# Kernel tuning notes

Measured on AMD Instinct MI355X. Metric: run time of the kernel, lower is better.

Reference implementation:

```python
import jax, jax.numpy as jnp
import numpy as np
import math

B, N, IN_DIM = 128, 100, 8
E, H, FF, L = 512, 8, 2048, 6
DH = E // H
MAX_STEPS = int(N * 1.5)
EPS = 1e-5

def _ln(x, g, b):
    mu = x.mean(-1, keepdims=True)
    var = ((x - mu) ** 2).mean(-1, keepdims=True)
    return (x - mu) / jnp.sqrt(var + EPS) * g + b

def _mha(q_in, k_in, v_in, wq, bq, wk, bk, wv, bv, wo, bo):
    Bq, Sq = q_in.shape[0], q_in.shape[1]
    q = (q_in @ wq + bq).reshape(Bq, Sq, H, DH)
    k = (k_in @ wk + bk).reshape(Bq, -1, H, DH)
    v = (v_in @ wv + bv).reshape(Bq, -1, H, DH)
    s = jnp.einsum('bqhd,bkhd->bhqk', q, k) / math.sqrt(DH)
    a = jax.nn.softmax(s, axis=-1)
    o = jnp.einsum('bhqk,bkhd->bqhd', a, v).reshape(Bq, Sq, E)
    return o @ wo + bo

def setup_inputs():
    key = jax.random.key(0)
    keys = iter(jax.random.split(key, 64))
    def nrm(shape, s=0.02):
        return jax.random.normal(next(keys), shape, jnp.float32) * s
    d = {}
    d['node_features'] = jax.random.normal(next(keys), (B, N, IN_DIM), jnp.float32)
    d['edge_weights'] = jax.random.uniform(next(keys), (B, N, N), jnp.float32)
    pos = np.arange(N)[:, None].astype(np.float32)
    div = np.exp(np.arange(0, E, 2).astype(np.float32) * (-math.log(10000.0) / E))
    pe = np.zeros((N, E), np.float32)
    pe[:, 0::2] = np.sin(pos * div); pe[:, 1::2] = np.cos(pos * div)
    d['pe'] = jnp.asarray(pe)
    d['in_w'] = nrm((IN_DIM, E)); d['in_b'] = jnp.zeros((E,), jnp.float32)
    for nm in ['enc_wq', 'enc_wk', 'enc_wv', 'enc_wo']:
        d[nm] = nrm((L, E, E))
    for nm in ['enc_bq', 'enc_bk', 'enc_bv', 'enc_bo']:
        d[nm] = jnp.zeros((L, E), jnp.float32)
    d['enc_w1'] = nrm((L, E, FF)); d['enc_b1'] = jnp.zeros((L, FF), jnp.float32)
    d['enc_w2'] = nrm((L, FF, E)); d['enc_b2'] = jnp.zeros((L, E), jnp.float32)
    d['enc_ln1g'] = jnp.ones((L, E), jnp.float32); d['enc_ln1b'] = jnp.zeros((L, E), jnp.float32)
    d['enc_ln2g'] = jnp.ones((L, E), jnp.float32); d['enc_ln2b'] = jnp.zeros((L, E), jnp.float32)
    d['lstm_wih'] = nrm((E, 4 * E)); d['lstm_whh'] = nrm((E, 4 * E))
    d['lstm_bih'] = jnp.zeros((4 * E,), jnp.float32); d['lstm_bhh'] = jnp.zeros((4 * E,), jnp.float32)
    for nm in ['dec_wq', 'dec_wk', 'dec_wv', 'dec_wo', 'dec_pw']:
        d[nm] = nrm((E, E))
    for nm in ['dec_bq', 'dec_bk', 'dec_bv', 'dec_bo', 'dec_pb']:
        d[nm] = jnp.zeros((E,), jnp.float32)
    d['dec_lng'] = jnp.ones((E,), jnp.float32); d['dec_lnb'] = jnp.zeros((E,), jnp.float32)
    d['shortcut_bonus'] = jnp.asarray(5.0, jnp.float32)
    d['revisit_penalty'] = jnp.asarray(-0.5, jnp.float32)
    d['done_w'] = nrm((E, 1)); d['done_b'] = jnp.zeros((1,), jnp.float32)
    return d

def _forward(node_features, edge_weights, pe, in_w, in_b, enc_wq, enc_bq, enc_wk, enc_bk, enc_wv, enc_bv, enc_wo, enc_bo, enc_w1, enc_b1, enc_w2, enc_b2, enc_ln1g, enc_ln1b, enc_ln2g, enc_ln2b, lstm_wih, lstm_whh, lstm_bih, lstm_bhh, dec_wq, dec_bq, dec_wk, dec_bk, dec_wv, dec_bv, dec_wo, dec_bo, dec_pw, dec_pb, dec_lng, dec_lnb, shortcut_bonus, revisit_penalty, done_w, done_b):
    # ---- Encoder (dropout = eval-mode identity) ----
    x = node_features @ in_w + in_b + pe[:N]
    for l in range(L):
        attn = _mha(x, x, x, enc_wq[l], enc_bq[l], enc_wk[l], enc_bk[l], enc_wv[l], enc_bv[l], enc_wo[l], enc_bo[l])
        x = _ln(x + attn, enc_ln1g[l], enc_ln1b[l])
        ff = jax.nn.relu(x @ enc_w1[l] + enc_b1[l]) @ enc_w2[l] + enc_b2[l]
        x = _ln(x + ff, enc_ln2g[l], enc_ln2b[l])
    node_emb = x  # [B, N, E]

    ar = jnp.arange(N)
    ew_to_first = edge_weights[:, :, 0]  # dist(mid -> node 0), [B, N]

    def step_fn(carry, step):
        h, c, ctx, visited, ucount, complete, all_vis, first, prev = carry
        # LSTMCell, torch gate order (i, f, g, o)
        gates = ctx @ lstm_wih + lstm_bih + h @ lstm_whh + lstm_bhh
        i_g, f_g, g_g, o_g = jnp.split(gates, 4, axis=-1)
        c2 = jax.nn.sigmoid(f_g) * c + jax.nn.sigmoid(i_g) * jnp.tanh(g_g)
        h2 = jax.nn.sigmoid(o_g) * jnp.tanh(c2)
        # greedy done-predictor: stop if sigmoid(logit) > 0.5 once tour can be closed
        done_p = jax.nn.sigmoid(h2 @ done_w + done_b)[:, 0]
        eligible = (~complete) & (ucount >= N) & (step >= N)
        complete = complete | (eligible & (done_p > 0.5))
        # DecoderStep: 1-query attention over node embeddings
        a = _mha(h2[:, None, :], node_emb, node_emb, dec_wq, dec_bq, dec_wk, dec_bk, dec_wv, dec_bv, dec_wo, dec_bo)[:, 0]
        a = _ln(a, dec_lng, dec_lnb)
        logits = a @ dec_pw + dec_pb
        scores = jnp.einsum('be,bne->bn', logits, node_emb)
        # revisit penalty while tour incomplete (vectorized masked_fill_)
        scores = jnp.where((~all_vis)[:, None] & visited, revisit_penalty, scores)
        # shortcut bonus once all nodes visited (vectorized gather over edge_weights)
        ew_prev = jnp.take_along_axis(edge_weights, prev[:, None, None], axis=1)[:, 0, :]  # [B, N] row dist(prev -> *)
        direct = ew_prev[:, :1]                      # dist(prev -> 0)
        via = ew_prev + ew_to_first                  # dist(prev -> mid) + dist(mid -> 0)
        bonus = jnp.where(via < direct, shortcut_bonus * (direct - via) / direct, 0.0)
        scores = scores + jnp.where(all_vis[:, None], bonus, 0.0)
        # completed tours: force return to first node
        scores = jnp.where(complete[:, None], -1e9, scores)
        scores = jnp.where(complete[:, None] & (ar[None, :] == first[:, None]), 100.0, scores)
        probs = jax.nn.softmax(scores, axis=1)
        curr = jnp.argmax(probs, axis=1).astype(jnp.int32)  # greedy selection
        logp = jnp.log(jnp.take_along_axis(probs, curr[:, None], 1)[:, 0] + 1e-10)
        first = jnp.where(step == 0, curr, first)
        # state updates (guarded by active, as in the torch per-batch loop)
        active = ~complete
        cur_mask = ar[None, :] == curr[:, None]
        newly = active & ~jnp.take_along_axis(visited, curr[:, None], 1)[:, 0]
        ucount = ucount + newly.astype(jnp.int32)
        visited = visited | (active[:, None] & cur_mask)
        all_vis = all_vis | (ucount >= N)
        ctx2 = jnp.take_along_axis(node_emb, curr[:, None, None], axis=1)[:, 0, :]
        return (h2, c2, ctx2, visited, ucount, complete, all_vis, first, curr), (curr, logp)

    carry0 = (jnp.zeros((B, E), jnp.float32), jnp.zeros((B, E), jnp.float32), node_emb.mean(1),
              jnp.zeros((B, N), bool), jnp.zeros((B,), jnp.int32),
              jnp.zeros((B,), bool), jnp.zeros((B,), bool),
              jnp.zeros((B,), jnp.int32), jnp.zeros((B,), jnp.int32))
    carry, (tours, logps) = jax.lax.scan(step_fn, carry0, jnp.arange(MAX_STEPS))
    complete, first = carry[5], carry[7]
    # final forced step (step == max_steps in torch): incomplete tours return to first node, logp = 0
    final_node = jnp.where(complete, jnp.int32(0), first)
    tours = jnp.concatenate([tours, final_node[None]], 0)                 # [MAX_STEPS+1, B]
    logps = jnp.concatenate([logps, jnp.zeros((1, B), jnp.float32)], 0)   # [MAX_STEPS+1, B]
    return logps, tours

def reference(node_features, edge_weights, pe, in_w, in_b, enc_wq, enc_bq, enc_wk, enc_bk, enc_wv, enc_bv, enc_wo, enc_bo, enc_w1, enc_b1, enc_w2, enc_b2, enc_ln1g, enc_ln1b, enc_ln2g, enc_ln2b, lstm_wih, lstm_whh, lstm_bih, lstm_bhh, dec_wq, dec_bq, dec_wk, dec_bk, dec_wv, dec_bv, dec_wo, dec_bo, dec_pw, dec_pb, dec_lng, dec_lnb, shortcut_bonus, revisit_penalty, done_w, done_b):
    return _forward(node_features, edge_weights, pe, in_w, in_b, enc_wq, enc_bq, enc_wk, enc_bk, enc_wv, enc_bv, enc_wo, enc_bo, enc_w1, enc_b1, enc_w2, enc_b2, enc_ln1g, enc_ln1b, enc_ln2g, enc_ln2b, lstm_wih, lstm_whh, lstm_bih, lstm_bhh, dec_wq, dec_bq, dec_wk, dec_bk, dec_wv, dec_bv, dec_wo, dec_bo, dec_pw, dec_pb, dec_lng, dec_lnb, shortcut_bonus, revisit_penalty, done_w, done_b)
```

## Files before the change

### kernel.cpp

```cpp
#include <hip/hip_runtime.h>
#include <math.h>

#define Bb 128
#define Nn 100
#define Ee 512
#define Hh 8
#define DHd 64
#define FFf 2048
#define Ll 6
#define STEPS 150

typedef _Float16 h8 __attribute__((ext_vector_type(8)));
typedef _Float16 h4 __attribute__((ext_vector_type(4)));
typedef float f4 __attribute__((ext_vector_type(4)));

template<bool RELU, bool BIAS, bool OUTF32, bool SPLITK>
__global__ __launch_bounds__(256) void mgemm_k(
    const _Float16* __restrict__ Ah, const _Float16* __restrict__ Al, int lda,
    const _Float16* __restrict__ Bh, const _Float16* __restrict__ Bl, int ldb,
    float* __restrict__ C, _Float16* __restrict__ Ch, _Float16* __restrict__ Cl,
    int ldc, const float* __restrict__ bias, int K, int kc, int Mtot)
{
  __shared__ _Float16 sm[4 * 5120];
  _Float16* sAh = sm;
// ... 96 lines not shown
  *(h4*)(Th + (size_t)(n0 + r) * K + k0 + c4) = hi;
  *(h4*)(Tl + (size_t)(n0 + r) * K + k0 + c4) = lo;
}

__global__ __launch_bounds__(256) void reduce4_k(
    const float* __restrict__ P, const float* __restrict__ bias, float* __restrict__ out)
{
  int idx = blockIdx.x * 256 + threadIdx.x;
  const size_t S = 3200ull * 512;
  float v = P[idx] + P[idx + S] + P[idx + 2 * S] + P[idx + 3 * S] + bias[idx & 511];
  out[idx] = v;
}

__global__ __launch_bounds__(256) void input_proj_k(
    const float* __restrict__ nf, const float* __restrict__ inw,
    const float* __restrict__ inb, const float* __restrict__ pe,
    float* __restrict__ x, _Float16* __restrict__ xh, _Float16* __restrict__ xl)
{
  int idx = blockIdx.x * 256 + threadIdx.x;
  int bn = idx >> 9, e = idx & 511;
  int n = bn - (bn / Nn) * Nn;
  const float* fr = nf + (size_t)bn * 8;
  float s = inb[e] + pe[(size_t)n * 512 + e];
#pragma unroll
  for (int i = 0; i < 8; ++i) s += fr[i] * inw[(size_t)i * 512 + e];
  x[idx] = s;
  _Float16 hh = (_Float16)s;
  xh[idx] = hh;
  xl[idx] = (_Float16)(s - (float)hh);
}

__global__ __launch_bounds__(256) void ln_k(
    const float* __restrict__ xin, const float* __restrict__ yin,
    const float* __restrict__ g, const float* __restrict__ bb,
    float* __restrict__ out, _Float16* __restrict__ oh, _Float16* __restrict__ ol)
{
  int row = blockIdx.x, t = threadIdx.x;
  __shared__ float red[256];
  size_t base = (size_t)row * 512;
  float v0 = xin[base + t] + yin[base + t];
  float v1 = xin[base + 256 + t] + yin[base + 256 + t];
  red[t] = v0 + v1;
  __syncthreads();
  for (int o = 128; o > 0; o >>= 1) { if (t < o) red[t] += red[t + o]; __syncthreads(); }
  float mu = red[0] * (1.f / 512.f);
  __syncthreads();
  float d0 = v0 - mu, d1 = v1 - mu;
  red[t] = d0 * d0 + d1 * d1;
  __syncthreads();
  for (int o = 128; o > 0; o >>= 1) { if (t < o) red[t] += red[t + o]; __syncthreads(); }
  float inv = 1.f / sqrtf(red[0] * (1.f / 512.f) + 1e-5f);
  float y0 = d0 * inv * g[t] + bb[t];
  float y1 = d1 * inv * g[t + 256] + bb[t + 256];
  out[base + t] = y0;
  out[base + 256 + t] = y1;
  _Float16 h0 = (_Float16)y0, h1 = (_Float16)y1;
  oh[base + t] = h0;           ol[base + t] = (_Float16)(y0 - (float)h0);
  oh[base + 256 + t] = h1;     ol[base + 256 + t] = (_Float16)(y1 - (float)h1);
}

__global__ __launch_bounds__(256) void enc_attn_k(
    const float* __restrict__ q, const float* __restrict__ k,
    const float* __restrict__ v, _Float16* __restrict__ oh, _Float16* __restrict__ ol)
{
  __shared__ __align__(16) float smem[14848];
  int bh = blockIdx.x; int b = bh >> 3, h = bh & 7;
  int t = threadIdx.x;
  float* qs = smem;
  float* kT = smem + 7616;
  float* p  = smem;
  const float* qg = q + ((size_t)b * Nn) * 512 + h * 64;
  const float* kg = k + ((size_t)b * Nn) * 512 + h * 64;
  const float* vg = v + ((size_t)b * Nn) * 512 + h * 64;
  for (int idx = t; idx < 6400; idx += 256) {
    int i = idx >> 6, d = idx & 63;
    qs[i * 68 + d]  = qg[(size_t)i * 512 + d];
    kT[d * 113 + i] = kg[(size_t)i * 512 + d];
  }
  __syncthreads();
  int ti = t >> 4, tj = t & 15;
  int i0 = ti * 7, j0 = tj * 7;
  float s[7][7];
#pragma unroll
  for (int r = 0; r < 7; ++r)
#pragma unroll
    for (int c = 0; c < 7; ++c) s[r][c] = 0.f;
  for (int kk = 0; kk < 64; ++kk) {
    float a[7], bb[7];
#pragma unroll
    for (int r = 0; r < 7; ++r) a[r] = qs[(i0 + r) * 68 + kk];
#pragma unroll
    for (int c = 0; c < 7; ++c) bb[c] = kT[kk * 113 + j0 + c];
#pragma unroll
    for (int r = 0; r < 7; ++r)
#pragma unroll
      for (int c = 0; c < 7; ++c) s[r][c] += a[r] * bb[c];
  }
  __syncthreads();
#pragma unroll
  for (int r = 0; r < 7; ++r)
#pragma unroll
    for (int c = 0; c < 7; ++c) {
      int i = i0 + r, j = j0 + c;
      if (i < Nn && j < Nn) p[i * 104 + j] = s[r][c] * 0.125f;
    }
  __syncthreads();
  int w = t >> 6, lane = t & 63;
  for (int i = w; i < Nn; i += 4) {
    float x0 = p[i * 104 + lane];
    float x1 = (lane < 36) ? p[i * 104 + 64 + lane] : -3.4e38f;
    float mx = fmaxf(x0, x1);
    for (int msk = 32; msk; msk >>= 1) mx = fmaxf(mx, __shfl_xor(mx, msk));
    float e0 = expf(x0 - mx);
    float e1 = (lane < 36) ? expf(x1 - mx) : 0.f;
    float ss = e0 + e1;
    for (int msk = 32; msk; msk >>= 1) ss += __shfl_xor(ss, msk);
    p[i * 104 + lane] = e0 / ss;
    if (lane < 36) p[i * 104 + 64 + lane] = e1 / ss;
  }
  __syncthreads();
  int d0 = tj * 4;
  float oa[7][4];
#pragma unroll
  for (int r = 0; r < 7; ++r)
#pragma unroll
    for (int c = 0; c < 4; ++c) oa[r][c] = 0.f;
  for (int j = 0; j < Nn; ++j) {
    float pr[7];
#pragma unroll
    for (int r = 0; r < 7; ++r) pr[r] = p[(i0 + r) * 104 + j];
    float4 vv = *(const float4*)(vg + (size_t)j * 512 + d0);
#pragma unroll
    for (int r = 0; r < 7; ++r) {
      oa[r][0] += pr[r] * vv.x; oa[r][1] += pr[r] * vv.y;
      oa[r][2] += pr[r] * vv.z; oa[r][3] += pr[r] * vv.w;
    }
  }
  size_t ob = ((size_t)b * Nn) * 512 + h * 64 + d0;
#pragma unroll
  for (int r = 0; r < 7; ++r)
    if (i0 + r < Nn) {
      h4 hv, lv;
#pragma unroll
      for (int c = 0; c < 4; ++c) {
        _Float16 hh = (_Float16)oa[r][c];
        hv[c] = hh;
        lv[c] = (_Float16)(oa[r][c] - (float)hh);
      }
      *(h4*)(oh + ob + (size_t)(i0 + r) * 512) = hv;
      *(h4*)(ol + ob + (size_t)(i0 + r) * 512) = lv;
    }
}

template<int BM, int BN, int BK, int TM, int TN>
__global__ __launch_bounds__(256) void gemm_k(
    const float* __restrict__ A, int lda,
    const float* __restrict__ B1, const float* __restrict__ B2, int splitB, int ldb,
    float* __restrict__ C, int ldc, int M, int N, int K, int kChunk)
{
  __shared__ __align__(16) float As[BK][BM + 4];
  __shared__ __align__(16) float Bs[BK][BN + 4];
  const int tid = threadIdx.x;
  const int m0 = blockIdx.y * BM;
  const int n0 = blockIdx.x * BN;
  const int k0 = blockIdx.z * kChunk;
  const int kEnd = k0 + kChunk;
  constexpr int TCOLS = BN / TN;
  const int tm = tid / TCOLS;
  const int tn = tid % TCOLS;
  float acc[TM][TN];
#pragma unroll
  for (int i = 0; i < TM; ++i)
#pragma unroll
    for (int j = 0; j < TN; ++j) acc[i][j] = 0.f;

  for (int kt = k0; kt < kEnd; kt += BK) {
    constexpr int A4 = BM * BK / 4;
    for (int c = tid; c < A4; c += 256) {
      int mm = c / (BK / 4);
      int k4 = (c % (BK / 4)) * 4;
      float4 av = *(const float4*)(A + (size_t)(m0 + mm) * lda + kt + k4);
      As[k4 + 0][mm] = av.x;
      As[k4 + 1][mm] = av.y;
      As[k4 + 2][mm] = av.z;
      As[k4 + 3][mm] = av.w;
    }
    constexpr int B4 = BK * BN / 4;
    for (int c = tid; c < B4; c += 256) {
      int kk = c / (BN / 4);
      int n4 = (c % (BN / 4)) * 4;
      int kgi = kt + kk;
      const float* Brow = (kgi < splitB) ? (B1 + (size_t)kgi * ldb)
                                         : (B2 + (size_t)(kgi - splitB) * ldb);
      *(float4*)&Bs[kk][n4] = *(const float4*)(Brow + n0 + n4);
    }
    __syncthreads();
#pragma unroll
    for (int kk = 0; kk < BK; ++kk) {
      float a[TM], b[TN];
#pragma unroll
      for (int i = 0; i < TM; ++i) a[i] = As[kk][tm * TM + i];
#pragma unroll
      for (int j = 0; j < TN; ++j) b[j] = Bs[kk][tn * TN + j];
#pragma unroll
      for (int i = 0; i < TM; ++i)
#pragma unroll
        for (int j = 0; j < TN; ++j)
          acc[i][j] += a[i] * b[j];
    }
    __syncthreads();
  }

  float* Cout = C + (size_t)blockIdx.z * (size_t)M * ldc;
#pragma unroll
  for (int i = 0; i < TM; ++i) {
    int m = m0 + tm * TM + i;
#pragma unroll
    for (int j = 0; j < TN; j += 4) {
      int n = n0 + tn * TN + j;
      float4 r;
      r.x = acc[i][j + 0]; r.y = acc[i][j + 1]; r.z = acc[i][j + 2]; r.w = acc[i][j + 3];
      *(float4*)(Cout + (size_t)m * ldc + n) = r;
    }
  }
}

__global__ __launch_bounds__(256) void init_k(
    const float* __restrict__ emb, float* __restrict__ ctxh, float* __restrict__ cbuf,
    int* visited, int* ucount, int* complete, int* allvis, int* first, int* prev,
    float* out)
{
  int b = blockIdx.x, t = threadIdx.x;
#pragma unroll
  for (int r = 0; r < 2; ++r) {
    int e = t + 256 * r;
    float s = 0.f;
    for (int i = 0; i < Nn; ++i) s += emb[((size_t)b * Nn + i) * 512 + e];
    ctxh[(size_t)b * 1024 + e] = s / 100.f;
    ctxh[(size_t)b * 1024 + 512 + e] = 0.f;
    cbuf[(size_t)b * 512 + e] = 0.f;
  }
  if (t < Nn) visited[b * Nn + t] = 0;
  if (t == 0) {
    ucount[b] = 0; complete[b] = 0; allvis[b] = 0; first[b] = 0; prev[b] = 0;
    out[150 * Bb + b] = 0.f;
  }
}

__device__ __forceinline__ float sigm(float x) { return 1.f / (1.f + expf(-x)); }

__global__ __launch_bounds__(256) void lstm_pw_k(
    const float* __restrict__ gP, const float* __restrict__ bih, const float* __restrict__ bhh,
    float* __restrict__ ctxh, float* __restrict__ cbuf,
    const float* __restrict__ done_w, const float* __restrict__ done_b,
    int* complete, const int* ucount, int step)
{
  int b = blockIdx.x, t = threadIdx.x;
  __shared__ float red[256];
  const float* g0 = gP + (size_t)b * 2048;
  const float* g1 = gP + 262144 + (size_t)b * 2048;
  float dsum = 0.f;
#pragma unroll
  for (int r = 0; r < 2; ++r) {
    int e = t + 256 * r;
    float ig = g0[e] + g1[e] + bih[e] + bhh[e];
    float fg = g0[e + 512] + g1[e + 512] + bih[e + 512] + bhh[e + 512];
    float gg = g0[e + 1024] + g1[e + 1024] + bih[e + 1024] + bhh[e + 1024];
    float og = g0[e + 1536] + g1[e + 1536] + bih[e + 1536] + bhh[e + 1536];
    float cprev = cbuf[(size_t)b * 512 + e];
    float c2 = sigm(fg) * cprev + sigm(ig) * tanhf(gg);
    float h2 = sigm(og) * tanhf(c2);
    cbuf[(size_t)b * 512 + e] = c2;
    ctxh[(size_t)b * 1024 + 512 + e] = h2;
    dsum += h2 * done_w[e];
  }
  red[t] = dsum; __syncthreads();
  for (int o = 128; o > 0; o >>= 1) { if (t < o) red[t] += red[t + o]; __syncthreads(); }
  if (t == 0) {
    float z = red[0] + done_b[0];
    if (!complete[b] && ucount[b] >= Nn && step >= Nn && z > 0.f) complete[b] = 1;
  }
}

__global__ __launch_bounds__(128) void dec_attn_k(
    const float* __restrict__ qP, const float* __restrict__ bq,
    const float* __restrict__ Kd, const float* __restrict__ Vd,
    float* __restrict__ o)
{
  int bh = blockIdx.x; int b = bh >> 3, h = bh & 7;
  int t = threadIdx.x;
  __shared__ float qh[64];
  __shared__ float p[100];
  __shared__ float red[128];
  if (t < 64) {
    float s = bq[h * 64 + t];
#pragma unroll
    for (int s8 = 0; s8 < 8; ++s8) s += qP[(size_t)s8 * 65536 + (size_t)b * 512 + h * 64 + t];
    qh[t] = s;
  }
  __syncthreads();
  float scv = -3.4e38f;
  if (t < Nn) {
    const float* kr = Kd + ((size_t)b * Nn + t) * 512 + h * 64;
    float s = 0.f;
#pragma unroll
    for (int d = 0; d < 64; ++d) s += qh[d] * kr[d];
    scv = s * 0.125f;
  }
  red[t] = scv; __syncthreads();
  for (int o2 = 64; o2 > 0; o2 >>= 1) { if (t < o2) red[t] = fmaxf(red[t], red[t + o2]); __syncthreads(); }
  float m = red[0]; __syncthreads();
  float ex = (t < Nn) ? expf(scv - m) : 0.f;
  red[t] = ex; __syncthreads();
  for (int o2 = 64; o2 > 0; o2 >>= 1) { if (t < o2) red[t] += red[t + o2]; __syncthreads(); }
  float Z = red[0];
  if (t < Nn) p[t] = ex / Z;
  __syncthreads();
  if (t < 64) {
    float acc = 0.f;
    const float* vr = Vd + (size_t)b * Nn * 512 + h * 64 + t;
    for (int j = 0; j < Nn; ++j) acc += p[j] * vr[(size_t)j * 512];
    o[(size_t)b * 512 + h * 64 + t] = acc;
  }
}

__global__ __launch_bounds__(256) void dec_ln_k(
    const float* __restrict__ woP, const float* __restrict__ bo,
    const float* __restrict__ g, const float* __restrict__ bb,
    float* __restrict__ out)
{
  int b = blockIdx.x, t = threadIdx.x;
  __shared__ float red[256];
  float v[2];
#pragma unroll
  for (int r = 0; r < 2; ++r) {
    int e = t + 256 * r;
    float s = bo[e];
#pragma unroll
    for (int s8 = 0; s8 < 8; ++s8) s += woP[(size_t)s8 * 65536 + (size_t)b * 512 + e];
    v[r] = s;
  }
  red[t] = v[0] + v[1]; __syncthreads();
  for (int o = 128; o > 0; o >>= 1) { if (t < o) red[t] += red[t + o]; __syncthreads(); }
  float mu = red[0] * (1.f / 512.f);
  __syncthreads();
  float d0 = v[0] - mu, d1 = v[1] - mu;
  red[t] = d0 * d0 + d1 * d1; __syncthreads();
  for (int o = 128; o > 0; o >>= 1) { if (t < o) red[t] += red[t + o]; __syncthreads(); }
  float inv = 1.f / sqrtf(red[0] * (1.f / 512.f) + 1e-5f);
  out[(size_t)b * 512 + t] = d0 * inv * g[t] + bb[t];
  out[(size_t)b * 512 + t + 256] = d1 * inv * g[t + 256] + bb[t + 256];
}

__global__ __launch_bounds__(256) void select_k(
    const float* __restrict__ pwP, const float* __restrict__ pb,
    const float* __restrict__ emb, const float* __restrict__ ew,
    int* visited, int* ucount, int* complete, int* allvis, int* first, int* prev,
    float* __restrict__ ctxh, float* __restrict__ out,
    const float* __restrict__ sb_p, const float* __restrict__ rp_p, int step)
{
  int b = blockIdx.x, t = threadIdx.x;
  __shared__ float logits[512];
  __shared__ float sc[128];
  __shared__ float red[256];
  __shared__ int redi[256];
#pragma unroll
  for (int r = 0; r < 2; ++r) {
    int e = t + 256 * r;
    float s = pb[e];
#pragma unroll
    for (int s8 = 0; s8 < 8; ++s8) s += pwP[(size_t)s8 * 65536 + (size_t)b * 512 + e];
    logits[e] = s;
  }
  __syncthreads();
  if (t < Nn) {
    const float* er = emb + ((size_t)b * Nn + t) * 512;
    float s = 0.f;
    for (int e = 0; e < 512; ++e) s += logits[e] * er[e];
    int av = allvis[b];
    if (!av && visited[b * Nn + t]) s = rp_p[0];
    if (av) {
      int pv = prev[b];
      float direct = ew[(size_t)b * 10000 + (size_t)pv * 100];
      float via = ew[(size_t)b * 10000 + (size_t)pv * 100 + t] + ew[(size_t)b * 10000 + (size_t)t * 100];
      if (via < direct) s += sb_p[0] * (direct - via) / direct;
    }
    if (complete[b]) s = (t == first[b]) ? 100.f : -1e9f;
    sc[t] = s;
  }
  __syncthreads();
  float vv = (t < Nn) ? sc[t] : -3.4e38f;
  int ii = (t < Nn) ? t : 0x7fffffff;
  red[t] = vv; redi[t] = ii;
  __syncthreads();
  for (int o = 128; o > 0; o >>= 1) {
    if (t < o) {
      float v2 = red[t + o]; int i2 = redi[t + o];
      if (v2 > red[t] || (v2 == red[t] && i2 < redi[t])) { red[t] = v2; redi[t] = i2; }
    }
    __syncthreads();
  }
  float m = red[0];
  int curr = redi[0];
  __syncthreads();
  float ex = (t < Nn) ? expf(sc[t] - m) : 0.f;
  red[t] = ex; __syncthreads();
  for (int o = 128; o > 0; o >>= 1) { if (t < o) red[t] += red[t + o]; __syncthreads(); }
  float Z = red[0];
  if (t == 0) {
    float pcur = expf(sc[curr] - m) / Z;
    out[step * Bb + b] = logf(pcur + 1e-10f);
    out[(151 + step) * Bb + b] = (float)curr;
    if (!complete[b]) {
      if (!visited[b * Nn + curr]) ucount[b] = ucount[b] + 1;
      visited[b * Nn + curr] = 1;
    }
    if (ucount[b] >= Nn) allvis[b] = 1;
    if (step == 0) first[b] = curr;
    prev[b] = curr;
  }
  const float* src = emb + ((size_t)b * Nn + curr) * 512;
  ctxh[(size_t)b * 1024 + t] = src[t];
  ctxh[(size_t)b * 1024 + t + 256] = src[t + 256];
}

__global__ void final_k(const int* complete, const int* first, float* out)
{
  int b = threadIdx.x;
  out[(151 + 150) * Bb + b] = complete[b] ? 0.f : (float)first[b];
}

extern "C" void kernel_launch(void* const* d_in, const int* in_sizes, int n_in,
                              void* d_out, int out_size, void* d_ws, size_t ws_size,
                              hipStream_t stream)
{
  const float* nf      = (const float*)d_in[0];
  const float* ew      = (const float*)d_in[1];
  const float* pe      = (const float*)d_in[2];
  const float* in_w    = (const float*)d_in[3];
  const float* in_b    = (const float*)d_in[4];
  const float* enc_wq  = (const float*)d_in[5];
  const float* enc_wk  = (const float*)d_in[6];
  const float* enc_wv  = (const float*)d_in[7];
  const float* enc_wo  = (const float*)d_in[8];
  const float* enc_bq  = (const float*)d_in[9];
  const float* enc_bk  = (const float*)d_in[10];
  const float* enc_bv  = (const float*)d_in[11];
  const float* enc_bo  = (const float*)d_in[12];
  const float* enc_w1  = (const float*)d_in[13];
  const float* enc_b1  = (const float*)d_in[14];
  const float* enc_w2  = (const float*)d_in[15];
  const float* enc_b2  = (const float*)d_in[16];
  const float* ln1g    = (const float*)d_in[17];
  const float* ln1b    = (const float*)d_in[18];
  const float* ln2g    = (const float*)d_in[19];
  const float* ln2b    = (const float*)d_in[20];
  const float* wih     = (const float*)d_in[21];
  const float* whh     = (const float*)d_in[22];
  const float* bih     = (const float*)d_in[23];
  const float* bhh     = (const float*)d_in[24];
  const float* dwq     = (const float*)d_in[25];
  const float* dwk     = (const float*)d_in[26];
  const float* dwv     = (const float*)d_in[27];
  const float* dwo     = (const float*)d_in[28];
  const float* dpw     = (const float*)d_in[29];
  const float* dbq     = (const float*)d_in[30];
  const float* dbk     = (const float*)d_in[31];
  const float* dbv     = (const float*)d_in[32];
  const float* dbo     = (const float*)d_in[33];
  const float* dpb     = (const float*)d_in[34];
  const float* dlng    = (const float*)d_in[35];
  const float* dlnb    = (const float*)d_in[36];
  const float* sbp     = (const float*)d_in[37];
  const float* rpp     = (const float*)d_in[38];
  const float* done_w  = (const float*)d_in[39];
  const float* done_b  = (const float*)d_in[40];
  float* out = (float*)d_out;

  const size_t SZ = 12800ull * 512;
  float* ws = (float*)d_ws;
  float* x   = ws;
  float* xq  = x + SZ;
  float* xk  = xq + SZ;
  float* xv  = xk + SZ;
  _Float16* xh = (_Float16*)(xv + SZ);
  _Float16* xl = xh + SZ;
  _Float16* oh = xl + SZ;
  _Float16* ol = oh + SZ;
  _Float16* wb = ol + SZ;
  _Float16* wqh = wb;               _Float16* wql = wqh + 262144;
  _Float16* wkh = wql + 262144;     _Float16* wkl = wkh + 262144;
  _Float16* wvh = wkl + 262144;     _Float16* wvl = wvh + 262144;
  _Float16* woh_ = wvl + 262144;    _Float16* wol_ = woh_ + 262144;
  _Float16* w1h = wol_ + 262144;    _Float16* w1l = w1h + 1048576;
  _Float16* w2h = w1l + 1048576;    _Float16* w2l = w2h + 1048576;
  float* ctxh   = (float*)(w2l + 1048576);
  float* cbuf   = ctxh + 131072;
  float* gatesP = cbuf + 65536;
  float* qP     = gatesP + 524288;
  float* woP    = qP + 524288;
  float* pwP    = woP + 524288;
  float* abuf   = pwP + 524288;
  float* dbuf   = abuf + 65536;
  int* ivis     = (int*)(dbuf + 65536);
  int* ucount   = ivis + 12800;
  int* complete = ucount + 128;
  int* allvis   = complete + 128;
  int* first    = allvis + 128;
  int* prev     = first + 128;

  input_proj_k<<<25600, 256, 0, stream>>>(nf, in_w, in_b, pe, x, xh, xl);

  for (int l = 0; l < Ll; ++l) {
    const float* wq = enc_wq + (size_t)l * 262144;
    const float* wk = enc_wk + (size_t)l * 262144;
    const float* wv = enc_wv + (size_t)l * 262144;
    const float* wo = enc_wo + (size_t)l * 262144;
    const float* bq = enc_bq + (size_t)l * 512;
    const float* bk = enc_bk + (size_t)l * 512;
    const float* bv = enc_bv + (size_t)l * 512;
    const float* bo = enc_bo + (size_t)l * 512;
    const float* w1 = enc_w1 + (size_t)l * 1048576;
    const float* b1 = enc_b1 + (size_t)l * 2048;
    const float* w2 = enc_w2 + (size_t)l * 1048576;
    const float* b2 = enc_b2 + (size_t)l * 512;

    wconv_k<<<dim3(16, 16), 256, 0, stream>>>(wq, 512, 512, wqh, wql);
    wconv_k<<<dim3(16, 16), 256, 0, stream>>>(wk, 512, 512, wkh, wkl);
    wconv_k<<<dim3(16, 16), 256, 0, stream>>>(wv, 512, 512, wvh, wvl);
    wconv_k<<<dim3(16, 16), 256, 0, stream>>>(wo, 512, 512, woh_, wol_);
    wconv_k<<<dim3(64, 16), 256, 0, stream>>>(w1, 512, 2048, w1h, w1l);
    wconv_k<<<dim3(16, 64), 256, 0, stream>>>(w2, 2048, 512, w2h, w2l);

    mgemm_k<false, true, true, false><<<dim3(4, 100), 256, 0, stream>>>(
        xh, xl, 512, wqh, wql, 512, xq, nullptr, nullptr, 512, bq, 512, 0, 0);
    mgemm_k<false, true, true, false><<<dim3(4, 100), 256, 0, stream>>>(
        xh, xl, 512, wkh, wkl, 512, xk, nullptr, nullptr, 512, bk, 512, 0, 0);
    mgemm_k<false, true, true, false><<<dim3(4, 100), 256, 0, stream>>>(
        xh, xl, 512, wvh, wvl, 512, xv, nullptr, nullptr, 512, bv, 512, 0, 0);
    enc_attn_k<<<1024, 256, 0, stream>>>(xq, xk, xv, oh, ol);
    mgemm_k<false, true, true, false><<<dim3(4, 100), 256, 0, stream>>>(
        oh, ol, 512, woh_, wol_, 512, xq, nullptr, nullptr, 512, bo, 512, 0, 0);
    ln_k<<<12800, 256, 0, stream>>>(x, xq, ln1g + l * 512, ln1b + l * 512, x, xh, xl);
    for (int c = 0; c < 4; ++c) {
      mgemm_k<true, true, false, false><<<dim3(16, 25), 256, 0, stream>>>(
          xh + (size_t)c * 3200 * 512, xl + (size_t)c * 3200 * 512, 512,
          w1h, w1l, 512, nullptr, oh, ol, 2048, b1, 512, 0, 0);
      mgemm_k<false, false, true, true><<<dim3(4, 25, 4), 256, 0, stream>>>(
          oh, ol, 2048, w2h, w2l, 2048, xv, nullptr, nullptr, 512,
          nullptr, 2048, 512, 3200);
      reduce4_k<<<6400, 256, 0, stream>>>(xv, b2, xq + (size_t)c * 3200 * 512);
    }
    ln_k<<<12800, 256, 0, stream>>>(x, xq, ln2g + l * 512, ln2b + l * 512, x, xh, xl);
  }

  wconv_k<<<dim3(16, 16), 256, 0, stream>>>(dwk, 512, 512, wqh, wql);
  wconv_k<<<dim3(16, 16), 256, 0, stream>>>(dwv, 512, 512, wkh, wkl);
  mgemm_k<false, true, true, false><<<dim3(4, 100), 256, 0, stream>>>(
      xh, xl, 512, wqh, wql, 512, xk, nullptr, nullptr, 512, dbk, 512, 0, 0);
  mgemm_k<false, true, true, false><<<dim3(4, 100), 256, 0, stream>>>(
      xh, xl, 512, wkh, wkl, 512, xv, nullptr, nullptr, 512, dbv, 512, 0, 0);
  init_k<<<128, 256, 0, stream>>>(x, ctxh, cbuf, ivis, ucount, complete, allvis, first, prev, out);

  for (int step = 0; step < STEPS; ++step) {
    gemm_k<32, 64, 16, 2, 4><<<dim3(32, 4, 2), 256, 0, stream>>>(
        ctxh, 1024, wih, whh, 512, 2048, gatesP, 2048, 128, 2048, 1024, 512);
    lstm_pw_k<<<128, 256, 0, stream>>>(gatesP, bih, bhh, ctxh, cbuf, done_w, done_b,
                                       complete, ucount, step);
    gemm_k<32, 64, 16, 2, 4><<<dim3(8, 4, 8), 256, 0, stream>>>(
        ctxh + 512, 1024, dwq, dwq, 1 << 30, 512, qP, 512, 128, 512, 512, 64);
    dec_attn_k<<<1024, 128, 0, stream>>>(qP, dbq, xk, xv, dbuf);
    gemm_k<32, 64, 16, 2, 4><<<dim3(8, 4, 8), 256, 0, stream>>>(
        dbuf, 512, dwo, dwo, 1 << 30, 512, woP, 512, 128, 512, 512, 64);
    dec_ln_k<<<128, 256, 0, stream>>>(woP, dbo, dlng, dlnb, abuf);
    gemm_k<32, 64, 16, 2, 4><<<dim3(8, 4, 8), 256, 0, stream>>>(
        abuf, 512, dpw, dpw, 1 << 30, 512, pwP, 512, 128, 512, 512, 64);
    select_k<<<128, 256, 0, stream>>>(pwP, dpb, x, ew, ivis, ucount, complete, allvis,
                                      first, prev, ctxh, out, sbp, rpp, step);
  }
  final_k<<<1, 128, 0, stream>>>(complete, first, out);
}
```

Measured before the change: 16.52 ms.

## Fuse decode loop into persistent kernel with software grid barrier

Replaces the per-step sequence of eight decoder kernel launches with a single persistent 256-block kernel that loops over all steps. Phases are separated by an atomic generation-counter grid barrier. This removes kernel launch and inter-kernel gaps for roughly 1200 launches. It relies on all blocks being co-resident and adds spin-barrier latency per phase.

Result: slower. 58.77 ms (+255.7%).

```diff
diff --git a/kernel.cpp b/kernel.cpp
--- a/kernel.cpp
+++ b/kernel.cpp
@@ -272,83 +272,10 @@
     }
 }
 
-template<int BM, int BN, int BK, int TM, int TN>
-__global__ __launch_bounds__(256) void gemm_k(
-    const float* __restrict__ A, int lda,
-    const float* __restrict__ B1, const float* __restrict__ B2, int splitB, int ldb,
-    float* __restrict__ C, int ldc, int M, int N, int K, int kChunk)
-{
-  __shared__ __align__(16) float As[BK][BM + 4];
-  __shared__ __align__(16) float Bs[BK][BN + 4];
-  const int tid = threadIdx.x;
-  const int m0 = blockIdx.y * BM;
-  const int n0 = blockIdx.x * BN;
-  const int k0 = blockIdx.z * kChunk;
-  const int kEnd = k0 + kChunk;
-  constexpr int TCOLS = BN / TN;
-  const int tm = tid / TCOLS;
-  const int tn = tid % TCOLS;
-  float acc[TM][TN];
-#pragma unroll
-  for (int i = 0; i < TM; ++i)
-#pragma unroll
-    for (int j = 0; j < TN; ++j) acc[i][j] = 0.f;
-
-  for (int kt = k0; kt < kEnd; kt += BK) {
-    constexpr int A4 = BM * BK / 4;
-    for (int c = tid; c < A4; c += 256) {
-      int mm = c / (BK / 4);
-      int k4 = (c % (BK / 4)) * 4;
-      float4 av = *(const float4*)(A + (size_t)(m0 + mm) * lda + kt + k4);
-      As[k4 + 0][mm] = av.x;
-      As[k4 + 1][mm] = av.y;
-      As[k4 + 2][mm] = av.z;
-      As[k4 + 3][mm] = av.w;
-    }
-    constexpr int B4 = BK * BN / 4;
-    for (int c = tid; c < B4; c += 256) {
-      int kk = c / (BN / 4);
-      int n4 = (c % (BN / 4)) * 4;
-      int kgi = kt + kk;
-      const float* Brow = (kgi < splitB) ? (B1 + (size_t)kgi * ldb)
-                                         : (B2 + (size_t)(kgi - splitB) * ldb);
-      *(float4*)&Bs[kk][n4] = *(const float4*)(Brow + n0 + n4);
-    }
-    __syncthreads();
-#pragma unroll
-    for (int kk = 0; kk < BK; ++kk) {
-      float a[TM], b[TN];
-#pragma unroll
-      for (int i = 0; i < TM; ++i) a[i] = As[kk][tm * TM + i];
-#pragma unroll
-      for (int j = 0; j < TN; ++j) b[j] = Bs[kk][tn * TN + j];
-#pragma unroll
-      for (int i = 0; i < TM; ++i)
-#pragma unroll
-        for (int j = 0; j < TN; ++j)
-          acc[i][j] += a[i] * b[j];
-    }
-    __syncthreads();
-  }
-
-  float* Cout = C + (size_t)blockIdx.z * (size_t)M * ldc;
-#pragma unroll
-  for (int i = 0; i < TM; ++i) {
-    int m = m0 + tm * TM + i;
-#pragma unroll
-    for (int j = 0; j < TN; j += 4) {
-      int n = n0 + tn * TN + j;
-      float4 r;
-      r.x = acc[i][j + 0]; r.y = acc[i][j + 1]; r.z = acc[i][j + 2]; r.w = acc[i][j + 3];
-      *(float4*)(Cout + (size_t)m * ldc + n) = r;
-    }
-  }
-}
-
 __global__ __launch_bounds__(256) void init_k(
     const float* __restrict__ emb, float* __restrict__ ctxh, float* __restrict__ cbuf,
     int* visited, int* ucount, int* complete, int* allvis, int* first, int* prev,
-    float* out)
+    float* out, unsigned* barp)
 {
   int b = blockIdx.x, t = threadIdx.x;
 #pragma unroll
@@ -364,190 +291,295 @@
   if (t == 0) {
     ucount[b] = 0; complete[b] = 0; allvis[b] = 0; first[b] = 0; prev[b] = 0;
     out[150 * Bb + b] = 0.f;
+    if (b == 0) { barp[0] = 0u; barp[1] = 0u; }
   }
 }
 
 __device__ __forceinline__ float sigm(float x) { return 1.f / (1.f + expf(-x)); }
 
-__global__ __launch_bounds__(256) void lstm_pw_k(
-    const float* __restrict__ gP, const float* __restrict__ bih, const float* __restrict__ bhh,
+__device__ __forceinline__ void gridbar(unsigned* cnt, unsigned* gen, int nb, int t)
+{
+  __syncthreads();
+  if (t == 0) {
+    unsigned g = __hip_atomic_load(gen, __ATOMIC_ACQUIRE, __HIP_MEMORY_SCOPE_AGENT);
+    __threadfence();
+    unsigned a = __hip_atomic_fetch_add(cnt, 1u, __ATOMIC_ACQ_REL, __HIP_MEMORY_SCOPE_AGENT);
+    if (a == (unsigned)(nb - 1)) {
+      __hip_atomic_store(cnt, 0u, __ATOMIC_RELAXED, __HIP_MEMORY_SCOPE_AGENT);
+      __hip_atomic_fetch_add(gen, 1u, __ATOMIC_ACQ_REL, __HIP_MEMORY_SCOPE_AGENT);
+    } else {
+      while (__hip_atomic_load(gen, __ATOMIC_ACQUIRE, __HIP_MEMORY_SCOPE_AGENT) == g) {
+        __builtin_amdgcn_s_sleep(1);
+      }
+    }
+  }
+  __syncthreads();
+}
+
+__device__ __forceinline__ void gemm_phase(
+    float (*As)[36], float (*Bs)[68], int t,
+    const float* __restrict__ A, int lda,
+    const float* __restrict__ B1, const float* __restrict__ B2, int splitB, int ldb,
+    float* __restrict__ C, int ldc, int M, int kChunk, int bx, int by, int bz)
+{
+  const int m0 = by * 32, n0 = bx * 64;
+  const int k0 = bz * kChunk, kEnd = k0 + kChunk;
+  const int tm = t >> 4, tn = t & 15;
+  float acc[2][4];
+#pragma unroll
+  for (int i = 0; i < 2; ++i)
+#pragma unroll
+    for (int j = 0; j < 4; ++j) acc[i][j] = 0.f;
+
+  for (int kt = k0; kt < kEnd; kt += 16) {
+    if (t < 128) {
+      int mm = t >> 2, k4 = (t & 3) * 4;
+      float4 av = *(const float4*)(A + (size_t)(m0 + mm) * lda + kt + k4);
+      As[k4 + 0][mm] = av.x;
+      As[k4 + 1][mm] = av.y;
+      As[k4 + 2][mm] = av.z;
+      As[k4 + 3][mm] = av.w;
+    }
+    {
+      int kk = t >> 4, n4 = (t & 15) * 4;
+      int kgi = kt + kk;
+      const float* Brow = (kgi < splitB) ? (B1 + (size_t)kgi * ldb)
+                                         : (B2 + (size_t)(kgi - splitB) * ldb);
+      *(float4*)&Bs[kk][n4] = *(const float4*)(Brow + n0 + n4);
+    }
+    __syncthreads();
+#pragma unroll
+    for (int kk = 0; kk < 16; ++kk) {
+      float a[2], b[4];
+      a[0] = As[kk][tm * 2 + 0];
+      a[1] = As[kk][tm * 2 + 1];
+#pragma unroll
+      for (int j = 0; j < 4; ++j) b[j] = Bs[kk][tn * 4 + j];
+#pragma unroll
+      for (int i = 0; i < 2; ++i)
+#pragma unroll
+        for (int j = 0; j < 4; ++j)
+          acc[i][j] += a[i] * b[j];
+    }
+    __syncthreads();
+  }
+
+  float* Cout = C + (size_t)bz * (size_t)M * ldc;
+#pragma unroll
+  for (int i = 0; i < 2; ++i) {
+    int m = m0 + tm * 2 + i;
+    int n = n0 + tn * 4;
+    float4 r;
+    r.x = acc[i][0]; r.y = acc[i][1]; r.z = acc[i][2]; r.w = acc[i][3];
+    *(float4*)(Cout + (size_t)m * ldc + n) = r;
+  }
+}
+
+__global__ __launch_bounds__(256) void decode_k(
+    const float* __restrict__ wih, const float* __restrict__ whh,
+    const float* __restrict__ bih, const float* __restrict__ bhh,
+    const float* __restrict__ dwq, const float* __restrict__ dbq,
+    const float* __restrict__ dwo, const float* __restrict__ dbo,
+    const float* __restrict__ dpw, const float* __restrict__ dpb,
+    const float* __restrict__ dlng, const float* __restrict__ dlnb,
+    const float* __restrict__ done_w, const float* __restrict__ done_b,
+    const float* __restrict__ emb, const float* __restrict__ ew,
+    const float* __restrict__ Kd, const float* __restrict__ Vd,
     float* __restrict__ ctxh, float* __restrict__ cbuf,
-    const float* __restrict__ done_w, const float* __restrict__ done_b,
-    int* complete, const int* ucount, int step)
-{
-  int b = blockIdx.x, t = threadIdx.x;
+    float* __restrict__ gatesP, float* __restrict__ qP,
+    float* __restrict__ woP, float* __restrict__ pwP,
+    float* __restrict__ abuf, float* __restrict__ dbuf,
+    int* visited, int* ucount, int* complete, int* allvis, int* first, int* prev,
+    float* __restrict__ out, const float* __restrict__ sb_p, const float* __restrict__ rp_p,
+    unsigned* barp)
+{
+  __shared__ __align__(16) float As[16][36];
+  __shared__ __align__(16) float Bs[16][68];
   __shared__ float red[256];
-  const float* g0 = gP + (size_t)b * 2048;
-  const float* g1 = gP + 262144 + (size_t)b * 2048;
-  float dsum = 0.f;
-#pragma unroll
-  for (int r = 0; r < 2; ++r) {
-    int e = t + 256 * r;
-    float ig = g0[e] + g1[e] + bih[e] + bhh[e];
-    float fg = g0[e + 512] + g1[e + 512] + bih[e + 512] + bhh[e + 512];
-    float gg = g0[e + 1024] + g1[e + 1024] + bih[e + 1024] + bhh[e + 1024];
-    float og = g0[e + 1536] + g1[e + 1536] + bih[e + 1536] + bhh[e + 1536];
-    float cprev = cbuf[(size_t)b * 512 + e];
-    float c2 = sigm(fg) * cprev + sigm(ig) * tanhf(gg);
-    float h2 = sigm(og) * tanhf(c2);
-    cbuf[(size_t)b * 512 + e] = c2;
-    ctxh[(size_t)b * 1024 + 512 + e] = h2;
-    dsum += h2 * done_w[e];
-  }
-  red[t] = dsum; __syncthreads();
-  for (int o = 128; o > 0; o >>= 1) { if (t < o) red[t] += red[t + o]; __syncthreads(); }
-  if (t == 0) {
-    float z = red[0] + done_b[0];
-    if (!complete[b] && ucount[b] >= Nn && step >= Nn && z > 0.f) complete[b] = 1;
-  }
-}
-
-__global__ __launch_bounds__(128) void dec_attn_k(
-    const float* __restrict__ qP, const float* __restrict__ bq,
-    const float* __restrict__ Kd, const float* __restrict__ Vd,
-    float* __restrict__ o)
-{
-  int bh = blockIdx.x; int b = bh >> 3, h = bh & 7;
-  int t = threadIdx.x;
-  __shared__ float qh[64];
-  __shared__ float p[100];
-  __shared__ float red[128];
-  if (t < 64) {
-    float s = bq[h * 64 + t];
-#pragma unroll
-    for (int s8 = 0; s8 < 8; ++s8) s += qP[(size_t)s8 * 65536 + (size_t)b * 512 + h * 64 + t];
-    qh[t] = s;
-  }
-  __syncthreads();
-  float scv = -3.4e38f;
-  if (t < Nn) {
-    const float* kr = Kd + ((size_t)b * Nn + t) * 512 + h * 64;
-    float s = 0.f;
-#pragma unroll
-    for (int d = 0; d < 64; ++d) s += qh[d] * kr[d];
-    scv = s * 0.125f;
-  }
-  red[t] = scv; __syncthreads();
-  for (int o2 = 64; o2 > 0; o2 >>= 1) { if (t < o2) red[t] = fmaxf(red[t], red[t + o2]); __syncthreads(); }
-  float m = red[0]; __syncthreads();
-  float ex = (t < Nn) ? expf(scv - m) : 0.f;
-  red[t] = ex; __syncthreads();
-  for (int o2 = 64; o2 > 0; o2 >>= 1) { if (t < o2) red[t] += red[t + o2]; __syncthreads(); }
-  float Z = red[0];
-  if (t < Nn) p[t] = ex / Z;
-  __syncthreads();
-  if (t < 64) {
-    float acc = 0.f;
-    const float* vr = Vd + (size_t)b * Nn * 512 + h * 64 + t;
-    for (int j = 0; j < Nn; ++j) acc += p[j] * vr[(size_t)j * 512];
-    o[(size_t)b * 512 + h * 64 + t] = acc;
-  }
-}
-
-__global__ __launch_bounds__(256) void dec_ln_k(
-    const float* __restrict__ woP, const float* __restrict__ bo,
-    const float* __restrict__ g, const float* __restrict__ bb,
-    float* __restrict__ out)
-{
-  int b = blockIdx.x, t = threadIdx.x;
-  __shared__ float red[256];
-  float v[2];
-#pragma unroll
-  for (int r = 0; r < 2; ++r) {
-    int e = t + 256 * r;
-    float s = bo[e];
-#pragma unroll
-    for (int s8 = 0; s8 < 8; ++s8) s += woP[(size_t)s8 * 65536 + (size_t)b * 512 + e];
-    v[r] = s;
-  }
-  red[t] = v[0] + v[1]; __syncthreads();
-  for (int o = 128; o > 0; o >>= 1) { if (t < o) red[t] += red[t + o]; __syncthreads(); }
-  float mu = red[0] * (1.f / 512.f);
-  __syncthreads();
-  float d0 = v[0] - mu, d1 = v[1] - mu;
-  red[t] = d0 * d0 + d1 * d1; __syncthreads();
-  for (int o = 128; o > 0; o >>= 1) { if (t < o) red[t] += red[t + o]; __syncthreads(); }
-  float inv = 1.f / sqrtf(red[0] * (1.f / 512.f) + 1e-5f);
-  out[(size_t)b * 512 + t] = d0 * inv * g[t] + bb[t];
-  out[(size_t)b * 512 + t + 256] = d1 * inv * g[t + 256] + bb[t + 256];
-}
-
-__global__ __launch_bounds__(256) void select_k(
-    const float* __restrict__ pwP, const float* __restrict__ pb,
-    const float* __restrict__ emb, const float* __restrict__ ew,
-    int* visited, int* ucount, int* complete, int* allvis, int* first, int* prev,
-    float* __restrict__ ctxh, float* __restrict__ out,
-    const float* __restrict__ sb_p, const float* __restrict__ rp_p, int step)
-{
-  int b = blockIdx.x, t = threadIdx.x;
-  __shared__ float logits[512];
-  __shared__ float sc[128];
-  __shared__ float red[256];
-  __shared__ int redi[256];
-#pragma unroll
-  for (int r = 0; r < 2; ++r) {
-    int e = t + 256 * r;
-    float s = pb[e];
-#pragma unroll
-    for (int s8 = 0; s8 < 8; ++s8) s += pwP[(size_t)s8 * 65536 + (size_t)b * 512 + e];
-    logits[e] = s;
-  }
-  __syncthreads();
-  if (t < Nn) {
-    const float* er = emb + ((size_t)b * Nn + t) * 512;
-    float s = 0.f;
-    for (int e = 0; e < 512; ++e) s += logits[e] * er[e];
-    int av = allvis[b];
-    if (!av && visited[b * Nn + t]) s = rp_p[0];
-    if (av) {
-      int pv = prev[b];
-      float direct = ew[(size_t)b * 10000 + (size_t)pv * 100];
-      float via = ew[(size_t)b * 10000 + (size_t)pv * 100 + t] + ew[(size_t)b * 10000 + (size_t)t * 100];
-      if (via < direct) s += sb_p[0] * (direct - via) / direct;
-    }
-    if (complete[b]) s = (t == first[b]) ? 100.f : -1e9f;
-    sc[t] = s;
-  }
-  __syncthreads();
-  float vv = (t < Nn) ? sc[t] : -3.4e38f;
-  int ii = (t < Nn) ? t : 0x7fffffff;
-  red[t] = vv; redi[t] = ii;
-  __syncthreads();
-  for (int o = 128; o > 0; o >>= 1) {
-    if (t < o) {
-      float v2 = red[t + o]; int i2 = redi[t + o];
-      if (v2 > red[t] || (v2 == red[t] && i2 < redi[t])) { red[t] = v2; redi[t] = i2; }
-    }
-    __syncthreads();
-  }
-  float m = red[0];
-  int curr = redi[0];
-  __syncthreads();
-  float ex = (t < Nn) ? expf(sc[t] - m) : 0.f;
-  red[t] = ex; __syncthreads();
-  for (int o = 128; o > 0; o >>= 1) { if (t < o) red[t] += red[t + o]; __syncthreads(); }
-  float Z = red[0];
-  if (t == 0) {
-    float pcur = expf(sc[curr] - m) / Z;
-    out[step * Bb + b] = logf(pcur + 1e-10f);
-    out[(151 + step) * Bb + b] = (float)curr;
-    if (!complete[b]) {
-      if (!visited[b * Nn + curr]) ucount[b] = ucount[b] + 1;
-      visited[b * Nn + curr] = 1;
-    }
-    if (ucount[b] >= Nn) allvis[b] = 1;
-    if (step == 0) first[b] = curr;
-    prev[b] = curr;
-  }
-  const float* src = emb + ((size_t)b * Nn + curr) * 512;
-  ctxh[(size_t)b * 1024 + t] = src[t];
-  ctxh[(size_t)b * 1024 + t + 256] = src[t + 256];
-}
-
-__global__ void final_k(const int* complete, const int* first, float* out)
-{
-  int b = threadIdx.x;
-  out[(151 + 150) * Bb + b] = complete[b] ? 0.f : (float)first[b];
+  __shared__ int   redi[256];
+  __shared__ float lgs[512];
+  __shared__ float scs[128];
+  __shared__ float qhs[64];
+  __shared__ float pvs[100];
+  const int bid = blockIdx.x;
+  const int t = threadIdx.x;
+  unsigned* bcnt = barp;
+  unsigned* bgen = barp + 1;
+
+  for (int step = 0; step < STEPS; ++step) {
+    gemm_phase(As, Bs, t, ctxh, 1024, wih, whh, 512, 2048,
+               gatesP, 2048, 128, 512, bid & 31, (bid >> 5) & 3, bid >> 7);
+    gridbar(bcnt, bgen, 256, t);
+
+    if (bid < 128) {
+      const int b = bid;
+      const float* g0 = gatesP + (size_t)b * 2048;
+      const float* g1 = gatesP + 262144 + (size_t)b * 2048;
+      float dsum = 0.f;
+#pragma unroll
+      for (int r = 0; r < 2; ++r) {
+        int e = t + 256 * r;
+        float ig = g0[e] + g1[e] + bih[e] + bhh[e];
+        float fg = g0[e + 512] + g1[e + 512] + bih[e + 512] + bhh[e + 512];
+        float gg = g0[e + 1024] + g1[e + 1024] + bih[e + 1024] + bhh[e + 1024];
+        float og = g0[e + 1536] + g1[e + 1536] + bih[e + 1536] + bhh[e + 1536];
+        float cprev = cbuf[(size_t)b * 512 + e];
+        float c2 = sigm(fg) * cprev + sigm(ig) * tanhf(gg);
+        float h2 = sigm(og) * tanhf(c2);
+        cbuf[(size_t)b * 512 + e] = c2;
+        ctxh[(size_t)b * 1024 + 512 + e] = h2;
+        dsum += h2 * done_w[e];
+      }
+      red[t] = dsum; __syncthreads();
+      for (int o = 128; o > 0; o >>= 1) { if (t < o) red[t] += red[t + o]; __syncthreads(); }
+      if (t == 0) {
+        float z = red[0] + done_b[0];
+        if (!complete[b] && ucount[b] >= Nn && step >= Nn && z > 0.f) complete[b] = 1;
+      }
+    }
+    gridbar(bcnt, bgen, 256, t);
+
+    gemm_phase(As, Bs, t, ctxh + 512, 1024, dwq, dwq, 1 << 30, 512,
+               qP, 512, 128, 64, bid & 7, (bid >> 3) & 3, bid >> 5);
+    gridbar(bcnt, bgen, 256, t);
+
+    for (int i = 0; i < 4; ++i) {
+      int bh = bid + 256 * i;
+      int b = bh >> 3, h = bh & 7;
+      if (t < 64) {
+        float s = dbq[h * 64 + t];
+#pragma unroll
+        for (int s8 = 0; s8 < 8; ++s8) s += qP[(size_t)s8 * 65536 + (size_t)b * 512 + h * 64 + t];
+        qhs[t] = s;
+      }
+      __syncthreads();
+      float scv = -3.4e38f;
+      if (t < Nn) {
+        const float* kr = Kd + ((size_t)b * Nn + t) * 512 + h * 64;
+        float s = 0.f;
+#pragma unroll
+        for (int d = 0; d < 64; ++d) s += qhs[d] * kr[d];
+        scv = s * 0.125f;
+      }
+      if (t < 128) red[t] = scv;
+      __syncthreads();
+      for (int o2 = 64; o2 > 0; o2 >>= 1) { if (t < o2) red[t] = fmaxf(red[t], red[t + o2]); __syncthreads(); }
+      float m = red[0]; __syncthreads();
+      float ex = (t < Nn) ? expf(scv - m) : 0.f;
+      if (t < 128) red[t] = ex;
+      __syncthreads();
+      for (int o2 = 64; o2 > 0; o2 >>= 1) { if (t < o2) red[t] += red[t + o2]; __syncthreads(); }
+      float Z = red[0];
+      if (t < Nn) pvs[t] = ex / Z;
+      __syncthreads();
+      if (t < 64) {
+        float acc = 0.f;
+        const float* vr = Vd + (size_t)b * Nn * 512 + h * 64 + t;
+        for (int j = 0; j < Nn; ++j) acc += pvs[j] * vr[(size_t)j * 512];
+        dbuf[(size_t)b * 512 + h * 64 + t] = acc;
+      }
+      __syncthreads();
+    }
+    gridbar(bcnt, bgen, 256, t);
+
+    gemm_phase(As, Bs, t, dbuf, 512, dwo, dwo, 1 << 30, 512,
+               woP, 512, 128, 64, bid & 7, (bid >> 3) & 3, bid >> 5);
+    gridbar(bcnt, bgen, 256, t);
+
+    if (bid < 128) {
+      const int b = bid;
+      float v[2];
+#pragma unroll
+      for (int r = 0; r < 2; ++r) {
+        int e = t + 256 * r;
+        float s = dbo[e];
+#pragma unroll
+        for (int s8 = 0; s8 < 8; ++s8) s += woP[(size_t)s8 * 65536 + (size_t)b * 512 + e];
+        v[r] = s;
+      }
+      red[t] = v[0] + v[1]; __syncthreads();
+      for (int o = 128; o > 0; o >>= 1) { if (t < o) red[t] += red[t + o]; __syncthreads(); }
+      float mu = red[0] * (1.f / 512.f);
+      __syncthreads();
+      float d0 = v[0] - mu, d1 = v[1] - mu;
+      red[t] = d0 * d0 + d1 * d1; __syncthreads();
+      for (int o = 128; o > 0; o >>= 1) { if (t < o) red[t] += red[t + o]; __syncthreads(); }
+      float inv = 1.f / sqrtf(red[0] * (1.f / 512.f) + 1e-5f);
+      abuf[(size_t)b * 512 + t] = d0 * inv * dlng[t] + dlnb[t];
+      abuf[(size_t)b * 512 + t + 256] = d1 * inv * dlng[t + 256] + dlnb[t + 256];
+    }
+    gridbar(bcnt, bgen, 256, t);
+
+    gemm_phase(As, Bs, t, abuf, 512, dpw, dpw, 1 << 30, 512,
+               pwP, 512, 128, 64, bid & 7, (bid >> 3) & 3, bid >> 5);
+    gridbar(bcnt, bgen, 256, t);
+
+    if (bid < 128) {
+      const int b = bid;
+#pragma unroll
+      for (int r = 0; r < 2; ++r) {
+        int e = t + 256 * r;
+        float s = dpb[e];
+#pragma unroll
+        for (int s8 = 0; s8 < 8; ++s8) s += pwP[(size_t)s8 * 65536 + (size_t)b * 512 + e];
+        lgs[e] = s;
+      }
+      __syncthreads();
+      if (t < Nn) {
+        const float* er = emb + ((size_t)b * Nn + t) * 512;
+        float s = 0.f;
+        for (int e = 0; e < 512; ++e) s += lgs[e] * er[e];
+        int av = allvis[b];
+        if (!av && visited[b * Nn + t]) s = rp_p[0];
+        if (av) {
+          int pv = prev[b];
+          float direct = ew[(size_t)b * 10000 + (size_t)pv * 100];
+          float via = ew[(size_t)b * 10000 + (size_t)pv * 100 + t] + ew[(size_t)b * 10000 + (size_t)t * 100];
+          if (via < direct) s += sb_p[0] * (direct - via) / direct;
+        }
+        if (complete[b]) s = (t == first[b]) ? 100.f : -1e9f;
+        scs[t] = s;
+      }
+      __syncthreads();
+      float vv = (t < Nn) ? scs[t] : -3.4e38f;
+      int ii = (t < Nn) ? t : 0x7fffffff;
+      red[t] = vv; redi[t] = ii;
+      __syncthreads();
+      for (int o = 128; o > 0; o >>= 1) {
+        if (t < o) {
+          float v2 = red[t + o]; int i2 = redi[t + o];
+          if (v2 > red[t] || (v2 == red[t] && i2 < redi[t])) { red[t] = v2; redi[t] = i2; }
+        }
+        __syncthreads();
+      }
+      float m = red[0];
+      int curr = redi[0];
+      __syncthreads();
+      float ex = (t < Nn) ? expf(scs[t] - m) : 0.f;
+      red[t] = ex; __syncthreads();
+      for (int o = 128; o > 0; o >>= 1) { if (t < o) red[t] += red[t + o]; __syncthreads(); }
+      float Z = red[0];
+      if (t == 0) {
+        float pcur = expf(scs[curr] - m) / Z;
+        out[step * Bb + b] = logf(pcur + 1e-10f);
+        out[(151 + step) * Bb + b] = (float)curr;
+        if (!complete[b]) {
+          if (!visited[b * Nn + curr]) ucount[b] = ucount[b] + 1;
+          visited[b * Nn + curr] = 1;
+        }
+        if (ucount[b] >= Nn) allvis[b] = 1;
+        if (step == 0) first[b] = curr;
+        prev[b] = curr;
+      }
+      const float* src = emb + ((size_t)b * Nn + curr) * 512;
+      ctxh[(size_t)b * 1024 + t] = src[t];
+      ctxh[(size_t)b * 1024 + t + 256] = src[t + 256];
+    }
+    gridbar(bcnt, bgen, 256, t);
+  }
+
+  if (bid == 0 && t < 128)
+    out[(151 + 150) * Bb + t] = complete[t] ? 0.f : (float)first[t];
 }
 
 extern "C" void kernel_launch(void* const* d_in, const int* in_sizes, int n_in,
@@ -628,6 +660,7 @@
   int* allvis   = complete + 128;
   int* first    = allvis + 128;
   int* prev     = first + 128;
+  unsigned* barp = (unsigned*)(prev + 128);
 
   input_proj_k<<<25600, 256, 0, stream>>>(nf, in_w, in_b, pe, x, xh, xl);
 
@@ -680,23 +713,13 @@
       xh, xl, 512, wqh, wql, 512, xk, nullptr, nullptr, 512, dbk, 512, 0, 0);
   mgemm_k<false, true, true, false><<<dim3(4, 100), 256, 0, stream>>>(
       xh, xl, 512, wkh, wkl, 512, xv, nullptr, nullptr, 512, dbv, 512, 0, 0);
-  init_k<<<128, 256, 0, stream>>>(x, ctxh, cbuf, ivis, ucount, complete, allvis, first, prev, out);
-
-  for (int step = 0; step < STEPS; ++step) {
-    gemm_k<32, 64, 16, 2, 4><<<dim3(32, 4, 2), 256, 0, stream>>>(
-        ctxh, 1024, wih, whh, 512, 2048, gatesP, 2048, 128, 2048, 1024, 512);
-    lstm_pw_k<<<128, 256, 0, stream>>>(gatesP, bih, bhh, ctxh, cbuf, done_w, done_b,
-                                       complete, ucount, step);
-    gemm_k<32, 64, 16, 2, 4><<<dim3(8, 4, 8), 256, 0, stream>>>(
-        ctxh + 512, 1024, dwq, dwq, 1 << 30, 512, qP, 512, 128, 512, 512, 64);
-    dec_attn_k<<<1024, 128, 0, stream>>>(qP, dbq, xk, xv, dbuf);
-    gemm_k<32, 64, 16, 2, 4><<<dim3(8, 4, 8), 256, 0, stream>>>(
-        dbuf, 512, dwo, dwo, 1 << 30, 512, woP, 512, 128, 512, 512, 64);
-    dec_ln_k<<<128, 256, 0, stream>>>(woP, dbo, dlng, dlnb, abuf);
-    gemm_k<32, 64, 16, 2, 4><<<dim3(8, 4, 8), 256, 0, stream>>>(
-        abuf, 512, dpw, dpw, 1 << 30, 512, pwP, 512, 128, 512, 512, 64);
-    select_k<<<128, 256, 0, stream>>>(pwP, dpb, x, ew, ivis, ucount, complete, allvis,
-                                      first, prev, ctxh, out, sbp, rpp, step);
-  }
-  final_k<<<1, 128, 0, stream>>>(complete, first, out);
-}
+  init_k<<<128, 256, 0, stream>>>(x, ctxh, cbuf, ivis, ucount, complete, allvis,
+                                  first, prev, out, barp);
+
+  decode_k<<<256, 256, 0, stream>>>(
+      wih, whh, bih, bhh, dwq, dbq, dwo, dbo, dpw, dpb, dlng, dlnb,
+      done_w, done_b, x, ew, xk, xv,
+      ctxh, cbuf, gatesP, qP, woP, pwP, abuf, dbuf,
+      ivis, ucount, complete, allvis, first, prev,
+      out, sbp, rpp, barp);
+}
```
